# Performance work log

Measured on AMD Instinct MI355X. Metric: run time of the kernel, lower is better.

The kernel has to match this reference:

```python
import jax, jax.numpy as jnp
import numpy as np

M = 2          # interp_dim
D = 4          # interp_degree
MESH_LOWER = np.array([0.0, 0.0], dtype=np.float32)
MESH_UPPER = np.array([1.0, 1.0], dtype=np.float32)
MESH_SIZE = np.array([64, 64], dtype=np.int32)   # coe grid = mesh_size*D+1 = [257, 257]


def _lagrange_basis(t):
    """t: [N, M] local coordinate in [0, D]; returns bases [N, M, D+1].
    L_j(t) = prod_{k != j} (t - k) / (j - k)."""
    ks = jnp.arange(D + 1, dtype=t.dtype)
    tk = t[..., None] - ks                       # [N, M, D+1]
    bs = []
    for j in range(D + 1):                       # small fixed loop over D+1=5 bases
        num = jnp.ones(t.shape, t.dtype)
        denom = 1.0
        for k in range(D + 1):
            if k != j:
                num = num * tk[..., k]
                denom *= float(j - k)
        bs.append(num / denom)
    return jnp.stack(bs, axis=-1)                # [N, M, D+1]


def setup_inputs() -> dict:
    key = jax.random.key(0)
    k1, k2 = jax.random.split(key)
    inputs = jax.random.uniform(k1, (2048, 2048, M), dtype=jnp.float32)  # points in [0,1)^2
    grid = tuple(int(s) * D + 1 for s in MESH_SIZE)                      # (257, 257)
    interp_coe = jax.random.normal(k2, grid, dtype=jnp.float32)
    return {"inputs": inputs, "interp_coe": interp_coe}


def reference(inputs, interp_coe):
    size = inputs.shape
    x = inputs.reshape(-1, M)                                   # [N, M]
    lower = jnp.asarray(MESH_LOWER, x.dtype)
    upper = jnp.asarray(MESH_UPPER, x.dtype)
    msize = jnp.asarray(MESH_SIZE.astype(np.float32), x.dtype)
    u = (x - lower) / (upper - lower) * msize                   # grid coordinates
    cell = jnp.clip(jnp.floor(u), 0.0, msize - 1.0)             # [N, M] element index
    t = (u - cell) * D                                          # local coord in [0, D]
    basis = _lagrange_basis(t)                                  # [N, M, D+1]
    base = cell.astype(jnp.int32) * D                           # [N, M] global node base index
    offs = jnp.arange(D + 1, dtype=jnp.int32)
    i0 = base[:, 0, None] + offs                                # [N, D+1]
    i1 = base[:, 1, None] + offs                                # [N, D+1]
    coe = interp_coe[i0[:, :, None], i1[:, None, :]]            # [N, D+1, D+1] gathered cell coes
    out = jnp.einsum('nij,ni,nj->n', coe, basis[:, 0], basis[:, 1])
    return out.reshape(size[:-1])
```

## Files before the change

kernel.cpp:

```cpp
#include <hip/hip_runtime.h>

#define NGRID 257
#define LDS_PITCH 260
#define LDS_BYTES (LDS_PITCH * NGRID * 2)
#define BLOCK 1024
#define GRID 256
#define ITERS 16

typedef _Float16 half2_t __attribute__((ext_vector_type(2)));
typedef _Float16 half4_t __attribute__((ext_vector_type(4)));
typedef float    f32x2  __attribute__((ext_vector_type(2)));

struct __attribute__((packed, aligned(4))) f4u { float x, y, z, w; };

__device__ __forceinline__ half2_t pack2(float a, float b) {
    return __builtin_bit_cast(half2_t, __builtin_amdgcn_cvt_pkrtz(a, b));
}

__device__ __forceinline__ float rowscale(int r) {
    return (r & 1) ? (-1.0f / 6.0f) : ((r & 2) ? 0.25f : (1.0f / 24.0f));
}

__device__ __forceinline__ float eval_pt(const _Float16* __restrict__ lds,
                                         float x0, float x1) {
    float u0 = x0 * 64.0f, u1 = x1 * 64.0f;
    int ic0 = (int)u0;
    int ic1 = (int)u1;
    f32x2 fr = { __builtin_amdgcn_fractf(u0), __builtin_amdgcn_fractf(u1) };

    const _Float16* base  = lds + (ic0 * 4) * LDS_PITCH + ic1 * 4;
    const _Float16* base2 = base + 2 * LDS_PITCH;

    half4_t lo0 = *(const half4_t*)(base);
    half4_t lo1 = *(const half4_t*)(base + LDS_PITCH);
    half4_t lo2 = *(const half4_t*)(base2);
    half4_t lo3 = *(const half4_t*)(base2 + LDS_PITCH);
    half4_t lo4 = *(const half4_t*)(base2 + 2 * LDS_PITCH);
    half2_t h0 = *(const half2_t*)(base + 4);
    half2_t h1 = *(const half2_t*)(base + LDS_PITCH + 4);
    half2_t h2 = *(const half2_t*)(base2 + 4);
    half2_t h3 = *(const half2_t*)(base2 + LDS_PITCH + 4);
    half2_t h4 = *(const half2_t*)(base2 + 2 * LDS_PITCH + 4);

    f32x2 f0 = fr * 4.0f;
    f32x2 f1 = f0 - 1.0f;
    f32x2 f2 = f0 - 2.0f;
    f32x2 f3 = f1 - 2.0f;
    f32x2 f4 = f0 - 4.0f;
    f32x2 p01 = f0 * f1;
    f32x2 p12 = f1 * f2;
    f32x2 p23 = f2 * f3;
    f32x2 p34 = f3 * f4;
    f32x2 n0 = p12 * p34;
    f32x2 t02 = f0 * f2;
    f32x2 n1 = t02 * p34;
    f32x2 n2 = p01 * p34;
    f32x2 t24 = f2 * f4;
    f32x2 n3 = p01 * t24;
    f32x2 n4 = p01 * p23;

    half2_t q01 = pack2(n0[1], n1[1]);
    half2_t q23 = pack2(n2[1], n3[1]);
    float b14 = n4[1];

    half4_t lo[5] = { lo0, lo1, lo2, lo3, lo4 };
    half2_t hi[5] = { h0, h1, h2, h3, h4 };
    float rd[5];
#pragma unroll
    for (int i = 0; i < 5; ++i) {
        half2_t xy = __builtin_shufflevector(lo[i], lo[i], 0, 1);
        half2_t zw = __builtin_shufflevector(lo[i], lo[i], 2, 3);
        float r = (float)hi[i][0] * b14;
        r = __builtin_amdgcn_fdot2(zw, q23, r, false);
        r = __builtin_amdgcn_fdot2(xy, q01, r, false);
        rd[i] = r;
    }
    float accA = n4[0] * rd[4];
    accA = fmaf(n0[0], rd[0], accA);
    accA = fmaf(n2[0], rd[2], accA);
    float accB = n1[0] * rd[1];
    accB = fmaf(n3[0], rd[3], accB);
    return accA + accB;
}

__launch_bounds__(BLOCK, 4)
__global__ void lagrange_kernel(const float* __restrict__ inputs,
                                const float* __restrict__ coe,
                                float* __restrict__ out,
                                int npts) {
    extern __shared__ _Float16 lds[];
    const int t = threadIdx.x;

#pragma unroll
    for (int k = 0; k < 16; ++k) {
        int g = t + k * BLOCK;
        int r = g >> 6;
        int c4 = (g & 63) << 2;
        f4u q = *(const f4u*)(coe + r * NGRID + c4);
        float rs = rowscale(r);
        half4_t h = { (_Float16)(q.x * (rs * (1.0f / 24.0f))),
                      (_Float16)(q.y * (rs * (-1.0f / 6.0f))),
                      (_Float16)(q.z * (rs * 0.25f)),
                      (_Float16)(q.w * (rs * (-1.0f / 6.0f))) };
        *(half4_t*)(lds + r * LDS_PITCH + c4) = h;
    }
    if (t < 64) {
        int c4 = t << 2;
        f4u q = *(const f4u*)(coe + 256 * NGRID + c4);
        const float rs = 1.0f / 24.0f;
        half4_t h = { (_Float16)(q.x * (rs * (1.0f / 24.0f))),
                      (_Float16)(q.y * (rs * (-1.0f / 6.0f))),
                      (_Float16)(q.z * (rs * 0.25f)),
                      (_Float16)(q.w * (rs * (-1.0f / 6.0f))) };
        *(half4_t*)(lds + 256 * LDS_PITCH + c4) = h;
    }
    if (t < NGRID) {
        float rs = rowscale(t);
        lds[t * LDS_PITCH + 256] = (_Float16)(coe[t * NGRID + 256] * (rs * (1.0f / 24.0f)));
    }
    __syncthreads();

    const float2* __restrict__ in2 = (const float2*)inputs;
    const int tid = blockIdx.x * BLOCK + t;
    const int stride = GRID * BLOCK;
    (void)npts;

    float2 w0 = in2[tid];
    float2 w1 = in2[tid + stride];
#pragma unroll
    for (int k = 0; k < ITERS; ++k) {
        float2 w2;
        if (k + 2 < ITERS) w2 = in2[tid + (k + 2) * stride];
        float r = eval_pt(lds, w0.x, w0.y);
        __builtin_nontemporal_store(r, &out[tid + k * stride]);
        w0 = w1;
        w1 = w2;
    }
}

extern "C" void kernel_launch(void* const* d_in, const int* in_sizes, int n_in,
                              void* d_out, int out_size, void* d_ws, size_t ws_size,
                              hipStream_t stream) {
    const float* inputs = (const float*)d_in[0];
    const float* coe    = (const float*)d_in[1];
    float* out = (float*)d_out;
    int npts = out_size;

    (void)hipFuncSetAttribute((const void*)lagrange_kernel,
                              hipFuncAttributeMaxDynamicSharedMemorySize,
                              LDS_BYTES);

    dim3 grid(GRID), block(BLOCK);
    hipLaunchKernelGGL(lagrange_kernel, grid, block, LDS_BYTES, stream,
                       inputs, coe, out, npts);
}
```

Before: 86.10 us.

## Repack LDS coefficient table to dense pitch with separate transposed edge-column table

Stores the main 256x256 fp16 coefficient block at a power-of-two pitch, plus a separate last row, a transposed table of the 5th column values per cell and a small corner array. Each point now does five 8-byte row loads and three dword loads instead of five 8-byte and five 4-byte loads, and the 5th column contribution is computed through packed dot products. The input prefetch is also moved ahead of the LDS fill, and two independent point streams are interleaved per iteration with deeper prefetch to raise ILP. The trade-offs are a rare branch for edge cells, more setup work, and a different bank-conflict pattern from the new pitch.

```diff
diff --git a/kernel.cpp b/kernel.cpp
--- a/kernel.cpp
+++ b/kernel.cpp
@@ -1,11 +1,14 @@
 #include <hip/hip_runtime.h>
 
 #define NGRID 257
-#define LDS_PITCH 260
-#define LDS_BYTES (LDS_PITCH * NGRID * 2)
 #define BLOCK 1024
 #define GRID 256
-#define ITERS 16
+#define OUTER 8
+
+#define OFF1_H  65536
+#define T_DW    32896
+#define S2_H    81792
+#define LDS_BYTES 163616
 
 typedef _Float16 half2_t __attribute__((ext_vector_type(2)));
 typedef _Float16 half4_t __attribute__((ext_vector_type(4)));
@@ -21,27 +24,7 @@
     return (r & 1) ? (-1.0f / 6.0f) : ((r & 2) ? 0.25f : (1.0f / 24.0f));
 }
 
-__device__ __forceinline__ float eval_pt(const _Float16* __restrict__ lds,
-                                         float x0, float x1) {
-    float u0 = x0 * 64.0f, u1 = x1 * 64.0f;
-    int ic0 = (int)u0;
-    int ic1 = (int)u1;
-    f32x2 fr = { __builtin_amdgcn_fractf(u0), __builtin_amdgcn_fractf(u1) };
-
-    const _Float16* base  = lds + (ic0 * 4) * LDS_PITCH + ic1 * 4;
-    const _Float16* base2 = base + 2 * LDS_PITCH;
-
-    half4_t lo0 = *(const half4_t*)(base);
-    half4_t lo1 = *(const half4_t*)(base + LDS_PITCH);
-    half4_t lo2 = *(const half4_t*)(base2);
-    half4_t lo3 = *(const half4_t*)(base2 + LDS_PITCH);
-    half4_t lo4 = *(const half4_t*)(base2 + 2 * LDS_PITCH);
-    half2_t h0 = *(const half2_t*)(base + 4);
-    half2_t h1 = *(const half2_t*)(base + LDS_PITCH + 4);
-    half2_t h2 = *(const half2_t*)(base2 + 4);
-    half2_t h3 = *(const half2_t*)(base2 + LDS_PITCH + 4);
-    half2_t h4 = *(const half2_t*)(base2 + 2 * LDS_PITCH + 4);
-
+__device__ __forceinline__ void nbasis(f32x2 fr, f32x2 n[5]) {
     f32x2 f0 = fr * 4.0f;
     f32x2 f1 = f0 - 1.0f;
     f32x2 f2 = f0 - 2.0f;
@@ -51,35 +34,76 @@
     f32x2 p12 = f1 * f2;
     f32x2 p23 = f2 * f3;
     f32x2 p34 = f3 * f4;
-    f32x2 n0 = p12 * p34;
-    f32x2 t02 = f0 * f2;
-    f32x2 n1 = t02 * p34;
-    f32x2 n2 = p01 * p34;
-    f32x2 t24 = f2 * f4;
-    f32x2 n3 = p01 * t24;
-    f32x2 n4 = p01 * p23;
-
-    half2_t q01 = pack2(n0[1], n1[1]);
-    half2_t q23 = pack2(n2[1], n3[1]);
-    float b14 = n4[1];
-
-    half4_t lo[5] = { lo0, lo1, lo2, lo3, lo4 };
-    half2_t hi[5] = { h0, h1, h2, h3, h4 };
+    n[0] = p12 * p34;
+    n[1] = (f0 * f2) * p34;
+    n[2] = p01 * p34;
+    n[3] = p01 * (f2 * f4);
+    n[4] = p01 * p23;
+}
+
+__device__ __forceinline__ float eval_pt(const _Float16* __restrict__ lds,
+                                         float x0, float x1) {
+    float u0 = x0 * 64.0f, u1 = x1 * 64.0f;
+    int i0 = (int)u0;
+    int i1 = (int)u1;
+    f32x2 fr = { __builtin_amdgcn_fractf(u0), __builtin_amdgcn_fractf(u1) };
+
+    const _Float16* mb = lds + (i0 << 10) + (i1 << 2);
+    half4_t l0 = *(const half4_t*)(mb);
+    half4_t l1 = *(const half4_t*)(mb + 256);
+    half4_t l2 = *(const half4_t*)(mb + 512);
+    half4_t l3 = *(const half4_t*)(mb + 768);
+    const _Float16* p4 = (i0 < 63) ? (mb + 1024) : (lds + OFF1_H + (i1 << 2));
+    half4_t l4 = *(const half4_t*)(p4);
+
+    const unsigned* tp = (const unsigned*)lds + T_DW + 125 * i1 + 2 * i0;
+    unsigned D0 = tp[0], D1 = tp[1], D2 = tp[2];
+
+    f32x2 n[5];
+    nbasis(fr, n);
+    half2_t q01 = pack2(n[0][1], n[1][1]);
+    half2_t q23 = pack2(n[2][1], n[3][1]);
+    half2_t pA  = pack2(n[0][0], n[1][0]);
+    half2_t pB  = pack2(n[2][0], n[3][0]);
+
+    half2_t C01 = __builtin_bit_cast(half2_t, D0);
+    half2_t C23 = __builtin_bit_cast(half2_t, D1);
+    _Float16 C4 = __builtin_bit_cast(half2_t, D2)[0];
+    if (__builtin_expect(i0 >= 62, 0)) {
+        _Float16 v[5];
+#pragma unroll
+        for (int i = 0; i < 5; ++i) {
+            int r = 4 * i0 + i;
+            const _Float16* p;
+            if (i1 < 63) p = (r < 256) ? (lds + (r << 8) + (i1 << 2) + 4)
+                                       : (lds + OFF1_H + (i1 << 2) + 4);
+            else         p = lds + S2_H + (r - 248);
+            v[i] = *p;
+        }
+        C01 = half2_t{ v[0], v[1] };
+        C23 = half2_t{ v[2], v[3] };
+        C4  = v[4];
+    }
+
+    float cs = (float)C4 * n[4][0];
+    cs = __builtin_amdgcn_fdot2(C23, pB, cs, false);
+    cs = __builtin_amdgcn_fdot2(C01, pA, cs, false);
+
+    half4_t lo[5] = { l0, l1, l2, l3, l4 };
     float rd[5];
 #pragma unroll
     for (int i = 0; i < 5; ++i) {
         half2_t xy = __builtin_shufflevector(lo[i], lo[i], 0, 1);
         half2_t zw = __builtin_shufflevector(lo[i], lo[i], 2, 3);
-        float r = (float)hi[i][0] * b14;
-        r = __builtin_amdgcn_fdot2(zw, q23, r, false);
-        r = __builtin_amdgcn_fdot2(xy, q01, r, false);
-        rd[i] = r;
-    }
-    float accA = n4[0] * rd[4];
-    accA = fmaf(n0[0], rd[0], accA);
-    accA = fmaf(n2[0], rd[2], accA);
-    float accB = n1[0] * rd[1];
-    accB = fmaf(n3[0], rd[3], accB);
+        rd[i] = __builtin_amdgcn_fdot2(xy, q01,
+                __builtin_amdgcn_fdot2(zw, q23, 0.0f, false), false);
+    }
+    float accA = n[4][0] * rd[4];
+    accA = fmaf(n[0][0], rd[0], accA);
+    accA = fmaf(n[2][0], rd[2], accA);
+    float accB = n[4][1] * cs;
+    accB = fmaf(n[1][0], rd[1], accB);
+    accB = fmaf(n[3][0], rd[3], accB);
     return accA + accB;
 }
 
@@ -90,6 +114,17 @@
                                 int npts) {
     extern __shared__ _Float16 lds[];
     const int t = threadIdx.x;
+    const int tid = blockIdx.x * BLOCK + t;
+    const int stride = GRID * BLOCK;
+    const float2* __restrict__ in2 = (const float2*)inputs;
+    (void)npts;
+
+    float2 a0 = in2[tid];
+    float2 a1 = in2[tid + stride];
+    float2 a2 = in2[tid + 2 * stride];
+    float2 b0 = in2[tid + OUTER * stride];
+    float2 b1 = in2[tid + (OUTER + 1) * stride];
+    float2 b2 = in2[tid + (OUTER + 2) * stride];
 
 #pragma unroll
     for (int k = 0; k < 16; ++k) {
@@ -102,7 +137,7 @@
                       (_Float16)(q.y * (rs * (-1.0f / 6.0f))),
                       (_Float16)(q.z * (rs * 0.25f)),
                       (_Float16)(q.w * (rs * (-1.0f / 6.0f))) };
-        *(half4_t*)(lds + r * LDS_PITCH + c4) = h;
+        *(half4_t*)(lds + (r << 8) + c4) = h;
     }
     if (t < 64) {
         int c4 = t << 2;
@@ -112,29 +147,43 @@
                       (_Float16)(q.y * (rs * (-1.0f / 6.0f))),
                       (_Float16)(q.z * (rs * 0.25f)),
                       (_Float16)(q.w * (rs * (-1.0f / 6.0f))) };
-        *(half4_t*)(lds + 256 * LDS_PITCH + c4) = h;
-    }
-    if (t < NGRID) {
-        float rs = rowscale(t);
-        lds[t * LDS_PITCH + 256] = (_Float16)(coe[t * NGRID + 256] * (rs * (1.0f / 24.0f)));
+        *(half4_t*)(lds + OFF1_H + c4) = h;
+    }
+#pragma unroll
+    for (int j = 0; j < 8; ++j) {
+        int idx = t + j * BLOCK;
+        if (idx < 8000) {
+            int c1 = idx & 63;
+            int d  = idx >> 6;
+            const float* src = coe + (2 * d) * NGRID + 4 * c1 + 4;
+            float va = src[0];
+            float vb = src[NGRID];
+            float rsa = (d & 1) ? 0.25f : (1.0f / 24.0f);
+            va *= rsa * (1.0f / 24.0f);
+            vb *= (-1.0f / 6.0f) * (1.0f / 24.0f);
+            ((unsigned*)lds)[T_DW + 125 * c1 + d] =
+                __builtin_bit_cast(unsigned, pack2(va, vb));
+        }
+    }
+    if (t < 9) {
+        int r = 248 + t;
+        lds[S2_H + t] = (_Float16)(coe[r * NGRID + 256] * (rowscale(r) * (1.0f / 24.0f)));
     }
     __syncthreads();
 
-    const float2* __restrict__ in2 = (const float2*)inputs;
-    const int tid = blockIdx.x * BLOCK + t;
-    const int stride = GRID * BLOCK;
-    (void)npts;
-
-    float2 w0 = in2[tid];
-    float2 w1 = in2[tid + stride];
-#pragma unroll
-    for (int k = 0; k < ITERS; ++k) {
-        float2 w2;
-        if (k + 2 < ITERS) w2 = in2[tid + (k + 2) * stride];
-        float r = eval_pt(lds, w0.x, w0.y);
-        __builtin_nontemporal_store(r, &out[tid + k * stride]);
-        w0 = w1;
-        w1 = w2;
+#pragma unroll
+    for (int k = 0; k < OUTER; ++k) {
+        float2 a3, b3;
+        if (k + 3 < OUTER) {
+            a3 = in2[tid + (k + 3) * stride];
+            b3 = in2[tid + (k + OUTER + 3) * stride];
+        }
+        float ra = eval_pt(lds, a0.x, a0.y);
+        float rb = eval_pt(lds, b0.x, b0.y);
+        __builtin_nontemporal_store(ra, &out[tid + k * stride]);
+        __builtin_nontemporal_store(rb, &out[tid + (k + OUTER) * stride]);
+        a0 = a1; a1 = a2; a2 = a3;
+        b0 = b1; b1 = b2; b2 = b3;
     }
 }
 
```

Measured after the change: 92.03 us (median of 2 runs). 1.07x slower.
